# Optimization experiments

Hardware: AMD Instinct MI355X
Metric: run time of the kernel (lower is better)

Reference implementation:

```python
import jax, jax.numpy as jnp
import numpy as np

HEADS, DIM_KEY, DIM_VALUE, DIM, N, B = 8, 64, 192, 1536, 2048, 2
SCALE = DIM_KEY ** -0.5


def setup_inputs() -> dict:
    key = jax.random.key(0)
    ks = jax.random.split(key, 8)
    s = 0.02
    return {
        "x": jax.random.normal(ks[0], (B, N, DIM), jnp.float32),
        "Wq": jax.random.normal(ks[1], (DIM, HEADS * DIM_KEY), jnp.float32) * s,
        "Wk": jax.random.normal(ks[2], (DIM, HEADS * DIM_KEY), jnp.float32) * s,
        "Wv": jax.random.normal(ks[3], (DIM, HEADS * DIM_VALUE), jnp.float32) * s,
        "Wo": jax.random.normal(ks[4], (HEADS * DIM_VALUE, DIM), jnp.float32) * s,
        "bo": jnp.zeros((DIM,), jnp.float32),
        "pos_embed": jax.random.normal(ks[5], (HEADS, N, DIM_KEY), jnp.float32) * s,
        "rel_content_bias": jax.random.normal(ks[6], (1, HEADS, 1, DIM_KEY), jnp.float32),
    }


def _split_heads(t, d):
    # [B, N, H*d] -> [B, H, N, d]
    b, n, _ = t.shape
    return t.reshape(b, n, HEADS, d).transpose(0, 2, 1, 3)


def reference(x, Wq, Wk, Wv, Wo, bo, pos_embed, rel_content_bias):
    q = _split_heads(x @ Wq, DIM_KEY) * SCALE          # [B,H,N,dk]
    k = _split_heads(x @ Wk, DIM_KEY)                  # [B,H,N,dk]
    v = _split_heads(x @ Wv, DIM_VALUE)                # [B,H,N,dv]
    q_biased = q + pos_embed[None] + rel_content_bias  # additive biases fused into Q
    logits = jnp.einsum('bhid,bhjd->bhij', q_biased, k)
    attn = jax.nn.softmax(logits, axis=-1)
    out = jnp.einsum('bhij,bhjd->bhid', attn, v)       # [B,H,N,dv]
    out = out.transpose(0, 2, 1, 3).reshape(x.shape[0], x.shape[1], HEADS * DIM_VALUE)
    return out @ Wo + bo
```

## Files before the change

kernel.cpp:

```cpp
#include <hip/hip_runtime.h>

#define BB    2
#define HN    8
#define NSEQ  2048
#define DIMM  1536
#define DKD   64
#define DVD   192
#define QCOLS 512
#define VCOLS 1536

typedef short short8 __attribute__((ext_vector_type(8)));
typedef float f32x4  __attribute__((ext_vector_type(4)));
typedef unsigned short ushortT;

static __device__ inline ushortT f2bf(float f) {
    unsigned u = __builtin_bit_cast(unsigned, f);
    u = (u + 0x7FFFu + ((u >> 16) & 1u)) >> 16;
    return (ushortT)u;
}

static __device__ inline void gl_lds16(const ushortT* g, ushortT* l) {
    __builtin_amdgcn_global_load_lds(
        (const __attribute__((address_space(1))) unsigned int*)g,
        (__attribute__((address_space(3))) unsigned int*)l, 16, 0, 0);
}

#define FENCE_VM0()    asm volatile("s_waitcnt vmcnt(0)" ::: "memory")
#define FENCE_VM12()   asm volatile("s_waitcnt vmcnt(12)" ::: "memory")
#define FENCE_LGKM0()  asm volatile("s_waitcnt lgkmcnt(0)" ::: "memory")
#define FENCE_SOFT()   asm volatile("" ::: "memory")

__global__ __launch_bounds__(256)
void prep_kernel(const float* __restrict__ x,
                 const float* __restrict__ Wq, const float* __restrict__ Wk,
                 const float* __restrict__ Wv, const float* __restrict__ Wo,
                 ushortT* __restrict__ xb, ushortT* __restrict__ wqkv,
                 ushortT* __restrict__ wo_t)
{
    __shared__ ushortT tt[32][33];
    const int b = blockIdx.x, tid = threadIdx.x;

    if (b < 3072) {
        const size_t idx = (size_t)b * 256 + tid;
        const float4* p = (const float4*)x + idx * 2;
        const float4 a = p[0], c = p[1];
        short8 v;
        v[0] = f2bf(a.x); v[1] = f2bf(a.y); v[2] = f2bf(a.z); v[3] = f2bf(a.w);
        v[4] = f2bf(c.x); v[5] = f2bf(c.y); v[6] = f2bf(c.z); v[7] = f2bf(c.w);
        *(short8*)(xb + idx * 8) = v;
        return;
    }

    const float* W; ushortT* Wt; int ncols, t;
    if (b < 3840)      { W = Wq; Wt = wqkv;                          ncols = QCOLS; t = b - 3072; }
    else if (b < 4608) { W = Wk; Wt = wqkv + (size_t)QCOLS * DIMM;   ncols = QCOLS; t = b - 3840; }
    else if (b < 6912) { W = Wv; Wt = wqkv + (size_t)2*QCOLS * DIMM; ncols = VCOLS; t = b - 4608; }
    else               { W = Wo; Wt = wo_t;                          ncols = DIMM;  t = b - 6912; }

    const int nbx = ncols >> 5;
    const int c0 = (t % nbx) * 32, k0 = (t / nbx) * 32;
    const int lx = tid & 31, ly = tid >> 5;
    #pragma unroll
    for (int r = 0; r < 4; r++)
        tt[ly + r * 8][lx] = f2bf(W[(size_t)(k0 + ly + r * 8) * ncols + c0 + lx]);
    __syncthreads();
    #pragma unroll
    for (int r = 0; r < 4; r++)
        Wt[(size_t)(c0 + ly + r * 8) * DIMM + k0 + lx] = tt[lx][ly + r * 8];
}

__global__ __launch_bounds__(256)
void gemm_kernel(const ushortT* __restrict__ A, const ushortT* __restrict__ Bt,
                 const float* __restrict__ bo,
                 const float* __restrict__ pos, const float* __restrict__ rcb,
                 ushortT* __restrict__ q_ws, ushortT* __restrict__ k_ws,
                 ushortT* __restrict__ v_ws, float* __restrict__ Cout, int mode)
{
    __shared__ ushortT As[128 * 64];
    __shared__ ushortT Bs[64 * 64];

    const int tid  = threadIdx.x;
    const int wave = tid >> 6, lane = tid & 63;
    const int quad = lane >> 4, l15 = lane & 15;
    const int m0 = blockIdx.y * 128, n0 = blockIdx.x * 64;

    const int sl_r = lane >> 3;
    const int sl_c = ((lane & 7) ^ sl_r) * 8;

    const ushortT* Ab = A  + (size_t)m0 * DIMM;
    const ushortT* Bb = Bt + (size_t)n0 * DIMM;

    f32x4 acc[2][4];
    #pragma unroll
    for (int i = 0; i < 2; i++)
        #pragma unroll
        for (int j = 0; j < 4; j++) acc[i][j] = (f32x4){0.f, 0.f, 0.f, 0.f};

    for (int k0 = 0; k0 < DIMM; k0 += 64) {
        #pragma unroll
        for (int t = 0; t < 4; t++) {
            const int g = wave * 4 + t;
            gl_lds16(Ab + (size_t)(g * 8 + sl_r) * DIMM + k0 + sl_c, &As[g * 512]);
        }
        #pragma unroll
        for (int t = 0; t < 2; t++) {
            const int g = wave * 2 + t;
            gl_lds16(Bb + (size_t)(g * 8 + sl_r) * DIMM + k0 + sl_c, &Bs[g * 512]);
        }
        __syncthreads();

        short8 af[2][2], bf[4][2];
        #pragma unroll
        for (int i = 0; i < 2; i++) {
            const int r = wave * 32 + i * 16 + l15;
            #pragma unroll
            for (int ks = 0; ks < 2; ks++)
                af[i][ks] = *(const short8*)&As[r * 64 + (((ks * 4 + quad) ^ (l15 & 7)) * 8)];
        }
        #pragma unroll
        for (int j = 0; j < 4; j++) {
            const int r = j * 16 + l15;
            #pragma unroll
            for (int ks = 0; ks < 2; ks++)
                bf[j][ks] = *(const short8*)&Bs[r * 64 + (((ks * 4 + quad) ^ (l15 & 7)) * 8)];
        }

        #pragma unroll
        for (int ks = 0; ks < 2; ks++)
            #pragma unroll
            for (int i = 0; i < 2; i++)
                #pragma unroll
                for (int j = 0; j < 4; j++)
                    acc[i][j] = __builtin_amdgcn_mfma_f32_16x16x32_bf16(af[i][ks], bf[j][ks], acc[i][j], 0, 0, 0);

        __syncthreads();
    }

    #pragma unroll
    for (int i = 0; i < 2; i++) {
        #pragma unroll
        for (int j = 0; j < 4; j++) {
            const int gcol = n0 + j * 16 + l15;
            #pragma unroll
            for (int r = 0; r < 4; r++) {
                const int grow = m0 + wave * 32 + i * 16 + quad * 4 + r;
                const float val = acc[i][j][r];
                if (mode == 1) {
                    Cout[(size_t)grow * DIMM + gcol] = val + bo[gcol];
                } else {
                    const int b = grow >> 11, n = grow & (NSEQ - 1);
                    if (gcol < QCOLS) {
                        const int h = gcol >> 6, d = gcol & 63;
                        q_ws[((size_t)(b * HN + h) * NSEQ + n) * DKD + d] =
                            f2bf((val * 0.125f + pos[((size_t)h * NSEQ + n) * DKD + d] + rcb[h * DKD + d])
                                 * 1.4426950408889634f);
                    } else if (gcol < 2 * QCOLS) {
                        const int c = gcol - QCOLS, h = c >> 6, d = c & 63;
                        k_ws[((size_t)(b * HN + h) * NSEQ + n) * DKD + d] = f2bf(val);
                    } else {
                        const int c = gcol - 2 * QCOLS, h = c / DVD, d = c - h * DVD;
                        const int p = (n & ~31) | (((n & 15) << 1) | ((n >> 4) & 1));
                        v_ws[((size_t)(b * HN + h) * DVD + d) * NSEQ + p] = f2bf(val);
                    }
                }
            }
        }
    }
}

#define PLD2 40
#define SHIFT2 28.8539008178f

__global__ __launch_bounds__(128)
void flash_kernel(const ushortT* __restrict__ q_ws, const ushortT* __restrict__ k_ws,
                  const ushortT* __restrict__ v_ws, ushortT* __restrict__ attn)
{
    __shared__ ushortT lds[16384];

    const int tid = threadIdx.x;
    const int wave = tid >> 6, lane = tid & 63;
    const int quad = lane >> 4, l15 = lane & 15;

    const int bh = blockIdx.x & 15;
    const int qt = blockIdx.x >> 4;
    const int n0 = qt * 32;
    const int b  = bh >> 3, h = bh & 7;

    const ushortT* kg = k_ws + (size_t)bh * NSEQ * DKD + (size_t)(wave * 1024) * DKD;
    const ushortT* vg = v_ws + (size_t)bh * DVD * NSEQ + wave * 1024;

    ushortT* st = lds + wave * 8192;
    ushortT* Pw = st;

    const int k_r = lane >> 3, k_c = ((lane & 7) ^ (k_r & 7)) * 8;
    const int v_r = lane >> 2;
    const int v_c = ((lane & 3) ^ ((v_r >> 1) & 3)) * 8;

    short8 qf[2][2];
    #pragma unroll
    for (int mt = 0; mt < 2; mt++)
        #pragma unroll
        for (int ks = 0; ks < 2; ks++)
            qf[mt][ks] = *(const short8*)(q_ws + ((size_t)bh * NSEQ + n0 + mt * 16 + l15) * DKD + ks * 32 + quad * 8);

    f32x4 o[2][12];
    #pragma unroll
    for (int mt = 0; mt < 2; mt++)
        #pragma unroll
        for (int nt = 0; nt < 12; nt++) o[mt][nt] = (f32x4){0.f, 0.f, 0.f, 0.f};

    float l_part[2][4];
    #pragma unroll
    for (int mt = 0; mt < 2; mt++)
        #pragma unroll
        for (int i = 0; i < 4; i++) l_part[mt][i] = 0.f;

    for (int kt0 = 0; kt0 < 1024; kt0 += 32) {
        FENCE_LGKM0();

        #pragma unroll
        for (int t = 0; t < 4; t++)
            gl_lds16(kg + (size_t)(kt0 + t * 8 + k_r) * DKD + k_c, st + t * 512);
        #pragma unroll
        for (int u = 0; u < 12; u++)
            gl_lds16(vg + (size_t)(u * 16 + v_r) * NSEQ + kt0 + v_c, st + 2048 + u * 512);

        FENCE_VM12();

        f32x4 s[2][2];
        #pragma unroll
        for (int mt = 0; mt < 2; mt++)
            #pragma unroll
            for (int nt = 0; nt < 2; nt++) s[mt][nt] = (f32x4){0.f, 0.f, 0.f, 0.f};
        __builtin_amdgcn_s_setprio(1);
        #pragma unroll
        for (int ks = 0; ks < 2; ks++)
            #pragma unroll
            for (int nt = 0; nt < 2; nt++) {
                const int key = nt * 16 + l15;
                short8 kf = *(const short8*)&st[key * 64 + (((ks * 4 + quad) ^ (key & 7)) * 8)];
                s[0][nt] = __builtin_amdgcn_mfma_f32_16x16x32_bf16(qf[0][ks], kf, s[0][nt], 0, 0, 0);
                s[1][nt] = __builtin_amdgcn_mfma_f32_16x16x32_bf16(qf[1][ks], kf, s[1][nt], 0, 0, 0);
            }
        __builtin_amdgcn_s_setprio(0);

        #pragma unroll
        for (int mt = 0; mt < 2; mt++)
            #pragma unroll
            for (int i = 0; i < 4; i++) {
                const float p0 = __builtin_amdgcn_exp2f(s[mt][0][i] - SHIFT2);
                const float p1 = __builtin_amdgcn_exp2f(s[mt][1][i] - SHIFT2);
                l_part[mt][i] += p0 + p1;
                unsigned pk;
                asm("v_cvt_pk_bf16_f32 %0, %1, %2" : "=v"(pk) : "v"(p0), "v"(p1));
                *(unsigned*)&Pw[(mt * 16 + quad * 4 + i) * PLD2 + 2 * l15] = pk;
            }

        FENCE_SOFT();

        short8 a[2];
        #pragma unroll
        for (int mt = 0; mt < 2; mt++)
            a[mt] = *(const short8*)&Pw[(mt * 16 + l15) * PLD2 + quad * 8];

        FENCE_VM0();

        __builtin_amdgcn_s_setprio(1);
        #pragma unroll
        for (int nt2 = 0; nt2 < 12; nt2++) {
            const int d = nt2 * 16 + l15;
            short8 vf = *(const short8*)&st[2048 + d * 32 + ((quad ^ ((l15 >> 1) & 3)) * 8)];
            o[0][nt2] = __builtin_amdgcn_mfma_f32_16x16x32_bf16(a[0], vf, o[0][nt2], 0, 0, 0);
            o[1][nt2] = __builtin_amdgcn_mfma_f32_16x16x32_bf16(a[1], vf, o[1][nt2], 0, 0, 0);
        }
        __builtin_amdgcn_s_setprio(0);
    }

    #pragma unroll
    for (int off = 1; off <= 8; off <<= 1)
        #pragma unroll
        for (int mt = 0; mt < 2; mt++)
            #pragma unroll
            for (int i = 0; i < 4; i++)
                l_part[mt][i] += __shfl_xor(l_part[mt][i], off, 64);

    __syncthreads();
    float* ox = (float*)lds;
    float* lx = (float*)(lds + 12288);
    if (wave == 1) {
        #pragma unroll
        for (int mt = 0; mt < 2; mt++)
            #pragma unroll
            for (int nt2 = 0; nt2 < 12; nt2++)
                #pragma unroll
                for (int i = 0; i < 4; i++)
                    ox[(((mt * 12 + nt2) * 4 + i) * 64) + lane] = o[mt][nt2][i];
        #pragma unroll
        for (int mt = 0; mt < 2; mt++)
            #pragma unroll
            for (int i = 0; i < 4; i++)
                lx[(mt * 4 + i) * 64 + lane] = l_part[mt][i];
    }
    __syncthreads();
    if (wave == 0) {
        float inv[2][4];
        #pragma unroll
        for (int mt = 0; mt < 2; mt++)
            #pragma unroll
            for (int i = 0; i < 4; i++)
                inv[mt][i] = 1.f / (l_part[mt][i] + lx[(mt * 4 + i) * 64 + lane]);
        #pragma unroll
        for (int mt = 0; mt < 2; mt++)
            #pragma unroll
            for (int nt2 = 0; nt2 < 12; nt2++)
                #pragma unroll
                for (int i = 0; i < 4; i++) {
                    const float v = o[mt][nt2][i] + ox[(((mt * 12 + nt2) * 4 + i) * 64) + lane];
                    const int n = n0 + mt * 16 + quad * 4 + i;
                    attn[((size_t)b * NSEQ + n) * DIMM + h * DVD + nt2 * 16 + l15] =
                        f2bf(v * inv[mt][i]);
                }
    }
}

extern "C" void kernel_launch(void* const* d_in, const int* in_sizes, int n_in,
                              void* d_out, int out_size, void* d_ws, size_t ws_size,
                              hipStream_t stream)
{
    const float* x   = (const float*)d_in[0];
    const float* Wq  = (const float*)d_in[1];
    const float* Wk  = (const float*)d_in[2];
    const float* Wv  = (const float*)d_in[3];
    const float* Wo  = (const float*)d_in[4];
    const float* bo  = (const float*)d_in[5];
    const float* pos = (const float*)d_in[6];
    const float* rcb = (const float*)d_in[7];
    float* out = (float*)d_out;

    ushortT* xb    = (ushortT*)d_ws;
    ushortT* wqkv  = xb    + (size_t)4096 * DIMM;
    ushortT* wo_t  = wqkv  + (size_t)(2 * QCOLS + VCOLS) * DIMM;
    ushortT* q_ws  = wo_t  + (size_t)DIMM * DIMM;
    ushortT* k_ws  = q_ws  + (size_t)BB * HN * NSEQ * DKD;
    ushortT* v_ws  = k_ws  + (size_t)BB * HN * NSEQ * DKD;
    ushortT* attnb = v_ws  + (size_t)BB * HN * NSEQ * DVD;

    prep_kernel<<<dim3(9216), dim3(256), 0, stream>>>(x, Wq, Wk, Wv, Wo, xb, wqkv, wo_t);

    gemm_kernel<<<dim3(40, 32), dim3(256), 0, stream>>>(xb, wqkv, bo, pos, rcb,
                                                        q_ws, k_ws, v_ws, nullptr, 0);
    flash_kernel<<<dim3(1024), dim3(128), 0, stream>>>(q_ws, k_ws, v_ws, attnb);
    gemm_kernel<<<dim3(24, 32), dim3(256), 0, stream>>>(attnb, wo_t, bo, pos, rcb,
                                                        q_ws, k_ws, v_ws, out, 1);
}
```

Baseline: 260.4 us.

## Rewrite GEMM as 256x256 double-buffered 8-wave pipelined kernel; drop flash setprio

The projection GEMMs move from 128x64 tiles with a load-sync-compute loop to 256x256 tiles run by 512 threads. Two LDS buffers are used, and the global-to-LDS stages are interleaved with quarter-tile MFMA phases under fine-grained barriers and waitcnt fences. This is meant to raise data reuse per loaded byte and hide memory latency behind MFMA work. The trade-off is far fewer blocks (160 and 96), which may underfill the device's CUs. The setprio hints in the flash kernel are also removed.

```diff
diff --git a/kernel.cpp b/kernel.cpp
--- a/kernel.cpp
+++ b/kernel.cpp
@@ -26,6 +26,7 @@
 }
 
 #define FENCE_VM0()    asm volatile("s_waitcnt vmcnt(0)" ::: "memory")
+#define FENCE_VM2()    asm volatile("s_waitcnt vmcnt(2)" ::: "memory")
 #define FENCE_VM12()   asm volatile("s_waitcnt vmcnt(12)" ::: "memory")
 #define FENCE_LGKM0()  asm volatile("s_waitcnt lgkmcnt(0)" ::: "memory")
 #define FENCE_SOFT()   asm volatile("" ::: "memory")
@@ -69,20 +70,23 @@
         Wt[(size_t)(c0 + ly + r * 8) * DIMM + k0 + lx] = tt[lx][ly + r * 8];
 }
 
-__global__ __launch_bounds__(256)
+#define NIT 12
+
+__global__ __launch_bounds__(512, 2)
 void gemm_kernel(const ushortT* __restrict__ A, const ushortT* __restrict__ Bt,
                  const float* __restrict__ bo,
                  const float* __restrict__ pos, const float* __restrict__ rcb,
                  ushortT* __restrict__ q_ws, ushortT* __restrict__ k_ws,
                  ushortT* __restrict__ v_ws, float* __restrict__ Cout, int mode)
 {
-    __shared__ ushortT As[128 * 64];
-    __shared__ ushortT Bs[64 * 64];
+    __shared__ ushortT As[2][256 * 64];
+    __shared__ ushortT Bs[2][256 * 64];
 
     const int tid  = threadIdx.x;
     const int wave = tid >> 6, lane = tid & 63;
     const int quad = lane >> 4, l15 = lane & 15;
-    const int m0 = blockIdx.y * 128, n0 = blockIdx.x * 64;
+    const int wr = wave >> 2, wc = wave & 3;
+    const int m0 = blockIdx.y * 256, n0 = blockIdx.x * 256;
 
     const int sl_r = lane >> 3;
     const int sl_c = ((lane & 7) ^ sl_r) * 8;
@@ -90,61 +94,126 @@
     const ushortT* Ab = A  + (size_t)m0 * DIMM;
     const ushortT* Bb = Bt + (size_t)n0 * DIMM;
 
-    f32x4 acc[2][4];
-    #pragma unroll
-    for (int i = 0; i < 2; i++)
+    f32x4 acc[8][4];
+    #pragma unroll
+    for (int i = 0; i < 8; i++)
         #pragma unroll
         for (int j = 0; j < 4; j++) acc[i][j] = (f32x4){0.f, 0.f, 0.f, 0.f};
 
-    for (int k0 = 0; k0 < DIMM; k0 += 64) {
-        #pragma unroll
-        for (int t = 0; t < 4; t++) {
-            const int g = wave * 4 + t;
-            gl_lds16(Ab + (size_t)(g * 8 + sl_r) * DIMM + k0 + sl_c, &As[g * 512]);
+    short8 af[4][2], bf[2][2];
+
+    auto STG = [&](ushortT* dst, const ushortT* gbase, int rowbase, int kcol) {
+        #pragma unroll
+        for (int i = 0; i < 2; i++) {
+            const int rg = rowbase + wave * 16 + i * 8;
+            gl_lds16(gbase + (size_t)(rg + sl_r) * DIMM + kcol + sl_c, dst + rg * 64);
         }
-        #pragma unroll
-        for (int t = 0; t < 2; t++) {
-            const int g = wave * 2 + t;
-            gl_lds16(Bb + (size_t)(g * 8 + sl_r) * DIMM + k0 + sl_c, &Bs[g * 512]);
-        }
-        __syncthreads();
-
-        short8 af[2][2], bf[4][2];
-        #pragma unroll
-        for (int i = 0; i < 2; i++) {
-            const int r = wave * 32 + i * 16 + l15;
-            #pragma unroll
-            for (int ks = 0; ks < 2; ks++)
-                af[i][ks] = *(const short8*)&As[r * 64 + (((ks * 4 + quad) ^ (l15 & 7)) * 8)];
-        }
-        #pragma unroll
-        for (int j = 0; j < 4; j++) {
-            const int r = j * 16 + l15;
-            #pragma unroll
-            for (int ks = 0; ks < 2; ks++)
-                bf[j][ks] = *(const short8*)&Bs[r * 64 + (((ks * 4 + quad) ^ (l15 & 7)) * 8)];
-        }
-
+    };
+    auto LDA = [&](const ushortT* buf, int mlo) {
+        #pragma unroll
+        for (int m = 0; m < 4; m++)
+            #pragma unroll
+            for (int ks = 0; ks < 2; ks++) {
+                const int r = wr * 128 + (mlo + m) * 16 + l15;
+                af[m][ks] = *(const short8*)&buf[r * 64 + (((ks * 4 + quad) ^ (l15 & 7)) * 8)];
+            }
+    };
+    auto LDB = [&](const ushortT* buf, int nlo) {
+        #pragma unroll
+        for (int n = 0; n < 2; n++)
+            #pragma unroll
+            for (int ks = 0; ks < 2; ks++) {
+                const int r = wc * 64 + (nlo + n) * 16 + l15;
+                bf[n][ks] = *(const short8*)&buf[r * 64 + (((ks * 4 + quad) ^ (l15 & 7)) * 8)];
+            }
+    };
+    auto MM = [&](int mlo, int nlo) {
+        __builtin_amdgcn_s_setprio(1);
         #pragma unroll
         for (int ks = 0; ks < 2; ks++)
             #pragma unroll
-            for (int i = 0; i < 2; i++)
+            for (int m = 0; m < 4; m++)
                 #pragma unroll
-                for (int j = 0; j < 4; j++)
-                    acc[i][j] = __builtin_amdgcn_mfma_f32_16x16x32_bf16(af[i][ks], bf[j][ks], acc[i][j], 0, 0, 0);
-
-        __syncthreads();
-    }
-
-    #pragma unroll
-    for (int i = 0; i < 2; i++) {
-        #pragma unroll
-        for (int j = 0; j < 4; j++) {
-            const int gcol = n0 + j * 16 + l15;
+                for (int n = 0; n < 2; n++)
+                    acc[mlo + m][nlo + n] = __builtin_amdgcn_mfma_f32_16x16x32_bf16(
+                        af[m][ks], bf[n][ks], acc[mlo + m][nlo + n], 0, 0, 0);
+        __builtin_amdgcn_s_setprio(0);
+    };
+
+    STG(Bs[0], Bb,   0, 0);
+    STG(Bs[0], Bb, 128, 0);
+    STG(As[0], Ab,   0, 0);
+    STG(As[0], Ab, 128, 0);
+    STG(Bs[1], Bb,   0, 64);
+    FENCE_VM2();
+    __builtin_amdgcn_s_barrier();
+
+    for (int it = 0; it < NIT; it++) {
+        const int kc1  = (2 * it + 1) * 64;
+        const int kcn0 = (2 * it + 2) * 64;
+        const int kcn1 = (2 * it + 3) * 64;
+        const bool more = (it + 1 < NIT);
+
+        LDA(As[0], 0); LDB(Bs[0], 0);
+        STG(As[1], Ab, 0, kc1);
+        __builtin_amdgcn_s_barrier(); FENCE_LGKM0();
+        MM(0, 0);
+        FENCE_SOFT(); __builtin_amdgcn_s_barrier();
+
+        LDA(As[0], 4);
+        STG(As[1], Ab, 128, kc1);
+        __builtin_amdgcn_s_barrier(); FENCE_LGKM0();
+        MM(4, 0);
+        FENCE_SOFT(); __builtin_amdgcn_s_barrier();
+
+        LDB(Bs[0], 2);
+        STG(Bs[1], Bb, 128, kc1);
+        __builtin_amdgcn_s_barrier(); FENCE_LGKM0();
+        MM(4, 2);
+        FENCE_SOFT(); __builtin_amdgcn_s_barrier();
+
+        LDA(As[0], 0);
+        if (more) STG(Bs[0], Bb, 0, kcn0);
+        __builtin_amdgcn_s_barrier(); FENCE_LGKM0();
+        MM(0, 2);
+        if (more) { FENCE_VM2(); } else { FENCE_VM0(); }
+        __builtin_amdgcn_s_barrier();
+
+        LDA(As[1], 0); LDB(Bs[1], 0);
+        if (more) STG(Bs[0], Bb, 128, kcn0);
+        __builtin_amdgcn_s_barrier(); FENCE_LGKM0();
+        MM(0, 0);
+        FENCE_SOFT(); __builtin_amdgcn_s_barrier();
+
+        LDA(As[1], 4);
+        if (more) STG(As[0], Ab, 0, kcn0);
+        __builtin_amdgcn_s_barrier(); FENCE_LGKM0();
+        MM(4, 0);
+        FENCE_SOFT(); __builtin_amdgcn_s_barrier();
+
+        LDB(Bs[1], 2);
+        if (more) STG(As[0], Ab, 128, kcn0);
+        __builtin_amdgcn_s_barrier(); FENCE_LGKM0();
+        MM(4, 2);
+        FENCE_SOFT(); __builtin_amdgcn_s_barrier();
+
+        LDA(As[1], 0);
+        if (more) STG(Bs[1], Bb, 0, kcn1);
+        __builtin_amdgcn_s_barrier(); FENCE_LGKM0();
+        MM(0, 2);
+        if (more) { FENCE_VM2(); }
+        __builtin_amdgcn_s_barrier();
+    }
+
+    #pragma unroll
+    for (int mi = 0; mi < 8; mi++) {
+        #pragma unroll
+        for (int nj = 0; nj < 4; nj++) {
+            const int gcol = n0 + wc * 64 + nj * 16 + l15;
             #pragma unroll
             for (int r = 0; r < 4; r++) {
-                const int grow = m0 + wave * 32 + i * 16 + quad * 4 + r;
-                const float val = acc[i][j][r];
+                const int grow = m0 + wr * 128 + mi * 16 + quad * 4 + r;
+                const float val = acc[mi][nj][r];
                 if (mode == 1) {
                     Cout[(size_t)grow * DIMM + gcol] = val + bo[gcol];
                 } else {
@@ -232,7 +301,6 @@
         for (int mt = 0; mt < 2; mt++)
             #pragma unroll
             for (int nt = 0; nt < 2; nt++) s[mt][nt] = (f32x4){0.f, 0.f, 0.f, 0.f};
-        __builtin_amdgcn_s_setprio(1);
         #pragma unroll
         for (int ks = 0; ks < 2; ks++)
             #pragma unroll
@@ -242,7 +310,6 @@
                 s[0][nt] = __builtin_amdgcn_mfma_f32_16x16x32_bf16(qf[0][ks], kf, s[0][nt], 0, 0, 0);
                 s[1][nt] = __builtin_amdgcn_mfma_f32_16x16x32_bf16(qf[1][ks], kf, s[1][nt], 0, 0, 0);
             }
-        __builtin_amdgcn_s_setprio(0);
 
         #pragma unroll
         for (int mt = 0; mt < 2; mt++)
@@ -265,7 +332,6 @@
 
         FENCE_VM0();
 
-        __builtin_amdgcn_s_setprio(1);
         #pragma unroll
         for (int nt2 = 0; nt2 < 12; nt2++) {
             const int d = nt2 * 16 + l15;
@@ -273,7 +339,6 @@
             o[0][nt2] = __builtin_amdgcn_mfma_f32_16x16x32_bf16(a[0], vf, o[0][nt2], 0, 0, 0);
             o[1][nt2] = __builtin_amdgcn_mfma_f32_16x16x32_bf16(a[1], vf, o[1][nt2], 0, 0, 0);
         }
-        __builtin_amdgcn_s_setprio(0);
     }
 
     #pragma unroll
@@ -347,9 +412,9 @@
 
     prep_kernel<<<dim3(9216), dim3(256), 0, stream>>>(x, Wq, Wk, Wv, Wo, xb, wqkv, wo_t);
 
-    gemm_kernel<<<dim3(40, 32), dim3(256), 0, stream>>>(xb, wqkv, bo, pos, rcb,
+    gemm_kernel<<<dim3(10, 16), dim3(512), 0, stream>>>(xb, wqkv, bo, pos, rcb,
                                                         q_ws, k_ws, v_ws, nullptr, 0);
     flash_kernel<<<dim3(1024), dim3(128), 0, stream>>>(q_ws, k_ws, v_ws, attnb);
-    gemm_kernel<<<dim3(24, 32), dim3(256), 0, stream>>>(attnb, wo_t, bo, pos, rcb,
-                                                        q_ws, k_ws, v_ws, out, 1);
-}
+    gemm_kernel<<<dim3(6, 16), dim3(512), 0, stream>>>(attnb, wo_t, bo, pos, rcb,
+                                                       q_ws, k_ws, v_ws, out, 1);
+}
```

New measurement: 324.8 us. +24.8%, slower.
